# Performance work log

Measured on AMD Instinct MI355X. Metric: run time of the kernel, lower is better.

The kernel has to match this reference:

```python
import jax, jax.numpy as jnp
import numpy as np
from jax import lax

DIM = 128
HEADS = 8
HEAD_DIM = DIM // HEADS
SR = 2
B, H, W = 2, 80, 80
SCALE = HEAD_DIM ** (-0.5)
BN_EPS = 1e-5


def _conv1x1(x, w, b):
    # x: (B,C,H,W), w: (O,C), b: (O,)
    return jnp.einsum('bchw,oc->bohw', x, w) + b[None, :, None, None]


def setup_inputs() -> dict:
    key = jax.random.key(0)
    ks = jax.random.split(key, 12)
    s = DIM ** -0.5
    x = jax.random.normal(ks[0], (B, DIM, H, W), dtype=jnp.float32)
    q_w = jax.random.normal(ks[1], (DIM, DIM), dtype=jnp.float32) * s
    q_b = jnp.zeros((DIM,), jnp.float32)
    k_w = jax.random.normal(ks[2], (DIM, DIM), dtype=jnp.float32) * s
    k_b = jnp.zeros((DIM,), jnp.float32)
    v_w = jax.random.normal(ks[3], (DIM, DIM), dtype=jnp.float32) * s
    v_b = jnp.zeros((DIM,), jnp.float32)
    sr_w = jax.random.normal(ks[4], (DIM, DIM, SR, SR), dtype=jnp.float32) * (s / SR)
    sr_b = jnp.zeros((DIM,), jnp.float32)
    bn_gamma = jnp.ones((DIM,), jnp.float32)
    bn_beta = jnp.zeros((DIM,), jnp.float32)
    bn_mean = jnp.zeros((DIM,), jnp.float32)
    bn_var = jnp.ones((DIM,), jnp.float32)
    proj_w = jax.random.normal(ks[5], (DIM, DIM), dtype=jnp.float32) * s
    proj_b = jnp.zeros((DIM,), jnp.float32)
    return dict(x=x, q_w=q_w, q_b=q_b, k_w=k_w, k_b=k_b, v_w=v_w, v_b=v_b,
                sr_w=sr_w, sr_b=sr_b, bn_gamma=bn_gamma, bn_beta=bn_beta,
                bn_mean=bn_mean, bn_var=bn_var, proj_w=proj_w, proj_b=proj_b)


def reference(x, q_w, q_b, k_w, k_b, v_w, v_b, sr_w, sr_b,
              bn_gamma, bn_beta, bn_mean, bn_var, proj_w, proj_b):
    b, c, h, w = x.shape
    n = h * w
    # q: (B,h,N,d)
    q = _conv1x1(x, q_w, q_b).reshape(b, HEADS, HEAD_DIM, n).transpose(0, 1, 3, 2)
    # spatial reduction: Conv2d(k=SR, s=SR) + BN(eval) + ReLU
    x_kv = lax.conv_general_dilated(x, sr_w, window_strides=(SR, SR),
                                    padding='VALID',
                                    dimension_numbers=('NCHW', 'OIHW', 'NCHW'))
    x_kv = x_kv + sr_b[None, :, None, None]
    inv = bn_gamma / jnp.sqrt(bn_var + BN_EPS)
    x_kv = x_kv * inv[None, :, None, None] + (bn_beta - bn_mean * inv)[None, :, None, None]
    x_kv = jax.nn.relu(x_kv)
    n_kv = x_kv.shape[2] * x_kv.shape[3]
    k = _conv1x1(x_kv, k_w, k_b).reshape(b, HEADS, HEAD_DIM, n_kv).transpose(0, 1, 3, 2)
    v = _conv1x1(x_kv, v_w, v_b).reshape(b, HEADS, HEAD_DIM, n_kv).transpose(0, 1, 3, 2)
    # explicit attention: (B,h,N,N_kv)
    attn = jnp.einsum('bhnd,bhmd->bhnm', q, k) * SCALE
    attn = jax.nn.softmax(attn, axis=-1)
    out = jnp.einsum('bhnm,bhmd->bhnd', attn, v)  # (B,h,N,d)
    # faithful to source layout: transpose(1,2) then reshape to (B,C,H,W)
    out = out.transpose(0, 2, 1, 3).reshape(b, c, h, w)
    out = _conv1x1(out, proj_w, proj_b)
    return out
```

## Files before the change

### kernel.cpp

```cpp
#include <hip/hip_runtime.h>
#include <hip/hip_bf16.h>
#include <cmath>

#define DIM 128
#define HEADS 8
#define NBATCH 2
#define NQ 6400
#define NKV 1600
#define NC 50
#define BN_EPS 1e-5f
#define LOG2E 1.4426950408889634f

typedef __bf16 bf16_t;
typedef __attribute__((ext_vector_type(8))) __bf16 bf16x8;
typedef __attribute__((ext_vector_type(16))) float f32x16;

union BF8U { bf16x8 v; unsigned u[4]; };

__device__ inline unsigned packbf2(float a, float b) {
  union { __hip_bfloat162 v; unsigned u; } r;
  r.v = __float22bfloat162_rn(make_float2(a, b));
  return r.u;
}

__device__ inline unsigned short f2bf(float v) {
  unsigned u = __float_as_uint(v);
  return (unsigned short)((u + 0x7FFFu + ((u >> 16) & 1u)) >> 16);
}

__device__ inline bf16x8 ldw8(const float* __restrict__ p) {
  float4 w0 = *(const float4*)p;
  float4 w1 = *(const float4*)(p + 4);
  BF8U r;
  r.u[0] = packbf2(w0.x, w0.y);
  r.u[1] = packbf2(w0.z, w0.w);
  r.u[2] = packbf2(w1.x, w1.y);
  r.u[3] = packbf2(w1.z, w1.w);
  return r.v;
}

__global__ __launch_bounds__(256) void mgemm_qsr(
    const float* __restrict__ x,
    const float* __restrict__ q_w, const float* __restrict__ q_b,
    const float* __restrict__ sr_w, const float* __restrict__ sr_b,
    const float* __restrict__ bng, const float* __restrict__ bnb,
    const float* __restrict__ bnm, const float* __restrict__ bnv,
    unsigned short* __restrict__ Qb, unsigned short* __restrict__ xkvb,
    float sl)
{
  int t = threadIdx.x;
  int ln = t & 31, hf = (t >> 5) & 1, wid = t >> 6;
  int b = blockIdx.y;
  int o = wid * 32 + ln;
  f32x16 acc = {};

  if (blockIdx.x < 200) {
    int s0 = blockIdx.x * 32;
    const float* ab = x + (size_t)b * DIM * NQ + s0 + ln;
    const float* brow = q_w + (size_t)o * 128 + hf * 8;
#pragma unroll
    for (int c0 = 0; c0 < 128; c0 += 16) {
      BF8U af;
#pragma unroll
      for (int jj = 0; jj < 4; ++jj)
        af.u[jj] = packbf2(ab[(size_t)(c0 + hf * 8 + 2 * jj) * NQ],
                           ab[(size_t)(c0 + hf * 8 + 2 * jj + 1) * NQ]);
      acc = __builtin_amdgcn_mfma_f32_32x32x16_bf16(af.v, ldw8(&brow[c0]), acc, 0, 0, 0);
    }
    float bv = q_b[o];
#pragma unroll
    for (int g = 0; g < 4; ++g)
#pragma unroll
      for (int j = 0; j < 4; ++j) {
        int s = s0 + 8 * g + 4 * hf + j;
        Qb[((size_t)b * NQ + s) * DIM + o] = f2bf((acc[4 * g + j] + bv) * sl);
      }
  } else {
    int s0 = (blockIdx.x - 200) * 32;
    int m = s0 + ln;
    int i = m / 40, jp = m % 40;
    const float* ab = x + (size_t)b * DIM * NQ + i * 160 + 2 * jp;
    const float* brow = sr_w + (size_t)o * 512 + hf * 8;
#pragma unroll 4
    for (int c0 = 0; c0 < 512; c0 += 16) {
      BF8U af;
#pragma unroll
      for (int jj = 0; jj < 4; ++jj) {
        int ca = c0 + hf * 8 + 2 * jj, cb = ca + 1;
        float va_ = ab[(size_t)(ca >> 2) * NQ + ((ca >> 1) & 1) * 80 + (ca & 1)];
        float vb_ = ab[(size_t)(cb >> 2) * NQ + ((cb >> 1) & 1) * 80 + (cb & 1)];
        af.u[jj] = packbf2(va_, vb_);
      }
      acc = __builtin_amdgcn_mfma_f32_32x32x16_bf16(af.v, ldw8(&brow[c0]), acc, 0, 0, 0);
    }
    float bv = sr_b[o];
    float inv = bng[o] / sqrtf(bnv[o] + BN_EPS);
    float b2 = bnb[o] - bnm[o] * inv;
#pragma unroll
    for (int g = 0; g < 4; ++g)
#pragma unroll
      for (int j = 0; j < 4; ++j) {
        int s = s0 + 8 * g + 4 * hf + j;
        float v = fmaxf((acc[4 * g + j] + bv) * inv + b2, 0.f);
        xkvb[((size_t)b * NKV + s) * DIM + o] = f2bf(v);
      }
  }
}

__global__ __launch_bounds__(256) void mgemm_kv(
    const bf16_t* __restrict__ xkvb,
    const float* __restrict__ k_w, const float* __restrict__ k_b,
    const float* __restrict__ v_w, const float* __restrict__ v_b,
    unsigned short* __restrict__ Kp, unsigned short* __restrict__ Vp)
{
  int t = threadIdx.x;
  int ln = t & 31, hf = (t >> 5) & 1, wid = t >> 6;
  int b = blockIdx.y;
  int isv = blockIdx.z;
  int s0 = blockIdx.x * 32;
  const float* W = isv ? v_w : k_w;
  int o = wid * 32 + ln;

  const bf16_t* arow = &xkvb[((size_t)b * NKV + s0 + ln) * DIM + hf * 8];
  const float* brow = W + (size_t)o * DIM + hf * 8;
  f32x16 acc = {};
#pragma unroll
  for (int c0 = 0; c0 < 128; c0 += 16) {
    bf16x8 af = *(const bf16x8*)&arow[c0];
    acc = __builtin_amdgcn_mfma_f32_32x32x16_bf16(af, ldw8(&brow[c0]), acc, 0, 0, 0);
  }

  int hloc = o >> 4, d = o & 15;
  if (isv) {
    float bv = v_b[o];
    size_t CB = (((size_t)b * HEADS + hloc) * NC + (s0 >> 5)) * 1024;
    uint4 w0, w1;
    w0.x = packbf2(acc[0] + bv, acc[1] + bv);
    w0.y = packbf2(acc[2] + bv, acc[3] + bv);
    w0.z = packbf2(acc[4] + bv, acc[5] + bv);
    w0.w = packbf2(acc[6] + bv, acc[7] + bv);
    w1.x = packbf2(acc[8] + bv, acc[9] + bv);
    w1.y = packbf2(acc[10] + bv, acc[11] + bv);
    w1.z = packbf2(acc[12] + bv, acc[13] + bv);
    w1.w = packbf2(acc[14] + bv, acc[15] + bv);
    *(uint4*)&Vp[CB + d * 16 + hf * 8] = w0;
    *(uint4*)&Vp[CB + 512 + d * 16 + hf * 8] = w1;
    {
      int h2 = t >> 5, pos = t & 31;
      size_t CB2 = (((size_t)b * HEADS + h2) * NC + (s0 >> 5)) * 1024;
      Vp[CB2 + 256 + ((pos & 16) ? 512 : 0) + (pos & 15)] = 0x3F80;
    }
  } else {
    float bv = k_b[o];
    size_t CB = (((size_t)b * HEADS + hloc) * NC + (s0 >> 5)) * 512;
#pragma unroll
    for (int g = 0; g < 4; ++g)
#pragma unroll
      for (int j = 0; j < 4; ++j) {
        int sl2 = 8 * g + 4 * hf + j;
        Kp[CB + sl2 * 16 + d] = f2bf(acc[4 * g + j] + bv);
      }
  }
}

__global__ __launch_bounds__(256, 8) void attn_split(
    const bf16_t* __restrict__ Qb, const bf16_t* __restrict__ Kp,
    const bf16_t* __restrict__ Vp, unsigned short* __restrict__ Pb,
    float* __restrict__ Lsum, int nsplit)
{
  const int t = threadIdx.x;
  const int ln = t & 31, hf = (t >> 5) & 1, wid = t >> 6;
  const int h = blockIdx.y;
  const int b = blockIdx.z & 1, quarter = blockIdx.z >> 1;
  const int q0 = blockIdx.x * 128 + wid * 32;
  const int base = NC / nsplit, rem = NC % nsplit;
  const int kcnt = base + (quarter < rem ? 1 : 0);
  const int kstart = quarter * base + (quarter < rem ? quarter : rem);
  const int slice = quarter * 2 + b;

  bf16x8 qf = *(const bf16x8*)&Qb[((size_t)b * NQ + q0 + ln) * DIM + h * 16 + hf * 8];
  const int bh = b * HEADS + h;
  const bf16_t* kc = &Kp[((size_t)bh * NC + kstart) * 512 + ln * 16 + hf * 8];
  const bf16_t* vc = &Vp[((size_t)bh * NC + kstart) * 1024 + ln * 16 + hf * 8];

  f32x16 acc = {};
  const f32x16 zero = {};

  for (int c = 0; c < kcnt; ++c) {
    bf16x8 kf = *(const bf16x8*)kc;
    bf16x8 va = *(const bf16x8*)vc;
    bf16x8 vb = *(const bf16x8*)(vc + 512);

    f32x16 S = __builtin_amdgcn_mfma_f32_32x32x16_bf16(kf, qf, zero, 0, 0, 0);

    BF8U f0, f1;
#pragma unroll
    for (int i = 0; i < 4; ++i) {
      f0.u[i] = packbf2(__builtin_amdgcn_exp2f(S[2 * i]),
                        __builtin_amdgcn_exp2f(S[2 * i + 1]));
      f1.u[i] = packbf2(__builtin_amdgcn_exp2f(S[8 + 2 * i]),
                        __builtin_amdgcn_exp2f(S[9 + 2 * i]));
    }

    acc = __builtin_amdgcn_mfma_f32_32x32x16_bf16(va, f0.v, acc, 0, 0, 0);
    acc = __builtin_amdgcn_mfma_f32_32x32x16_bf16(vb, f1.v, acc, 0, 0, 0);
    kc += 512; vc += 1024;
  }

  unsigned short* prow =
      &Pb[(size_t)slice * (NQ * DIM) + (size_t)(q0 + ln) * DIM + h * 16 + 4 * hf];
  uint2 w0, w1;
  w0.x = packbf2(acc[0], acc[1]); w0.y = packbf2(acc[2], acc[3]);
  w1.x = packbf2(acc[4], acc[5]); w1.y = packbf2(acc[6], acc[7]);
  *(uint2*)&prow[0] = w0;
  *(uint2*)&prow[8] = w1;
  if (!hf)
    Lsum[(size_t)slice * (HEADS * NQ) + (size_t)h * NQ + q0 + ln] = acc[8];
}

__global__ __launch_bounds__(256) void proj_comb(
    const unsigned short* __restrict__ Pb, const float* __restrict__ Lsum,
    const float* __restrict__ p_w, const float* __restrict__ p_b,
    float* __restrict__ Out, int nsplit)
{
  __shared__ unsigned short As[32][136];
  int t = threadIdx.x;
  int b = blockIdx.y;
  int s0 = blockIdx.x * 32;

  {
    int tx = t & 31, cg = t >> 5;
#pragma unroll
    for (int it = 0; it < 16; ++it) {
      int c = cg * 16 + it;
      int f = c * NQ + s0 + tx;
      int n = f >> 7, hh = (f >> 4) & 7;
      float ps = 0.f, L = 0.f;
      for (int qq = 0; qq < nsplit; ++qq) {
        int sl2 = qq * 2 + b;
        ps += __uint_as_float((unsigned)Pb[(size_t)sl2 * (NQ * DIM) + f] << 16);
        L += Lsum[(size_t)sl2 * (HEADS * NQ) + (size_t)hh * NQ + n];
      }
      As[tx][c] = f2bf(ps / L);
    }
  }
  __syncthreads();

  int ln = t & 31, hf = (t >> 5) & 1, wid = t >> 6;
  int o = wid * 32 + ln;
  const float* brow = p_w + (size_t)o * DIM + hf * 8;
  const unsigned short* arow = &As[ln][hf * 8];
  f32x16 acc = {};
#pragma unroll
  for (int c0 = 0; c0 < 128; c0 += 16) {
    bf16x8 af = *(const bf16x8*)&arow[c0];
    acc = __builtin_amdgcn_mfma_f32_32x32x16_bf16(af, ldw8(&brow[c0]), acc, 0, 0, 0);
  }
  float bv = p_b[o];
  float* obase = &Out[((size_t)b * DIM + o) * NQ + s0 + 4 * hf];
#pragma unroll
  for (int g = 0; g < 4; ++g) {
    float4 r;
    r.x = acc[4 * g + 0] + bv; r.y = acc[4 * g + 1] + bv;
    r.z = acc[4 * g + 2] + bv; r.w = acc[4 * g + 3] + bv;
    *(float4*)&obase[8 * g] = r;
  }
}

extern "C" void kernel_launch(void* const* d_in, const int* in_sizes, int n_in,
                              void* d_out, int out_size, void* d_ws, size_t ws_size,
                              hipStream_t stream)
{
  const float* x    = (const float*)d_in[0];
  const float* q_w  = (const float*)d_in[1];
  const float* q_b  = (const float*)d_in[2];
  const float* k_w  = (const float*)d_in[3];
  const float* k_b  = (const float*)d_in[4];
  const float* v_w  = (const float*)d_in[5];
  const float* v_b  = (const float*)d_in[6];
  const float* sr_w = (const float*)d_in[7];
  const float* sr_b = (const float*)d_in[8];
  const float* bng  = (const float*)d_in[9];
  const float* bnb  = (const float*)d_in[10];
  const float* bnm  = (const float*)d_in[11];
  const float* bnv  = (const float*)d_in[12];
  const float* p_w  = (const float*)d_in[13];
  const float* p_b  = (const float*)d_in[14];
  float* out = (float*)d_out;

  const int nsplit = (ws_size >= (size_t)5120000 * 4) ? 4 : 2;

  float* ws = (float*)d_ws;
  bf16_t* Pb   = (bf16_t*)ws;
  bf16_t* xkvb = (bf16_t*)ws;
  size_t off = (size_t)nsplit * 819200;
  bf16_t* Qb = (bf16_t*)(ws + off);   off += 819200;
  bf16_t* Kp = (bf16_t*)(ws + off);   off += 204800;
  bf16_t* Vp = (bf16_t*)(ws + off);   off += 409600;
  float* Lsum = ws + off;

  const float sl = 0.25f * LOG2E;

  mgemm_qsr<<<dim3(250, NBATCH), dim3(256), 0, stream>>>(
      x, q_w, q_b, sr_w, sr_b, bng, bnb, bnm, bnv,
      (unsigned short*)Qb, (unsigned short*)xkvb, sl);

  mgemm_kv<<<dim3(NKV / 32, NBATCH, 2), dim3(256), 0, stream>>>(
      xkvb, k_w, k_b, v_w, v_b, (unsigned short*)Kp, (unsigned short*)Vp);

  attn_split<<<dim3(NQ / 128, HEADS, 2 * nsplit), dim3(256), 0, stream>>>(
      Qb, Kp, Vp, (unsigned short*)Pb, Lsum, nsplit);

  proj_comb<<<dim3(200, NBATCH), dim3(256), 0, stream>>>(
      (const unsigned short*)Pb, Lsum, p_w, p_b, out, nsplit);
}
```

Baseline: 168.6 us.

## Stage Q-proj input via LDS, vectorize SR loads, prefetch next KV chunk in attention

The Q projection branch now loads the x tile cooperatively with float4 reads, converts it to bf16 into shared memory, and then reads MFMA A-fragments as 16-byte LDS loads. This replaces scattered strided scalar global loads. The spatial-reduction branch merges each adjacent pixel pair into one float2 load. The attention loop software-prefetches the next chunk's K/V fragments into registers to hide global latency, which costs extra registers and adds a barrier in the projection kernel.

```diff
diff --git a/kernel.cpp b/kernel.cpp
--- a/kernel.cpp
+++ b/kernel.cpp
@@ -48,6 +48,7 @@
     unsigned short* __restrict__ Qb, unsigned short* __restrict__ xkvb,
     float sl)
 {
+  __shared__ __align__(16) unsigned short As[32][136];
   int t = threadIdx.x;
   int ln = t & 31, hf = (t >> 5) & 1, wid = t >> 6;
   int b = blockIdx.y;
@@ -56,16 +57,25 @@
 
   if (blockIdx.x < 200) {
     int s0 = blockIdx.x * 32;
-    const float* ab = x + (size_t)b * DIM * NQ + s0 + ln;
+    const float* xb = x + (size_t)b * DIM * NQ + s0;
+#pragma unroll
+    for (int it = 0; it < 4; ++it) {
+      int idx = t + it * 256;
+      int c = idx >> 3, s4 = (idx & 7) * 4;
+      float4 v = *(const float4*)&xb[(size_t)c * NQ + s4];
+      As[s4 + 0][c] = f2bf(v.x);
+      As[s4 + 1][c] = f2bf(v.y);
+      As[s4 + 2][c] = f2bf(v.z);
+      As[s4 + 3][c] = f2bf(v.w);
+    }
+    __syncthreads();
+
     const float* brow = q_w + (size_t)o * 128 + hf * 8;
+    const unsigned short* arow = &As[ln][hf * 8];
 #pragma unroll
     for (int c0 = 0; c0 < 128; c0 += 16) {
-      BF8U af;
-#pragma unroll
-      for (int jj = 0; jj < 4; ++jj)
-        af.u[jj] = packbf2(ab[(size_t)(c0 + hf * 8 + 2 * jj) * NQ],
-                           ab[(size_t)(c0 + hf * 8 + 2 * jj + 1) * NQ]);
-      acc = __builtin_amdgcn_mfma_f32_32x32x16_bf16(af.v, ldw8(&brow[c0]), acc, 0, 0, 0);
+      bf16x8 af = *(const bf16x8*)&arow[c0];
+      acc = __builtin_amdgcn_mfma_f32_32x32x16_bf16(af, ldw8(&brow[c0]), acc, 0, 0, 0);
     }
     float bv = q_b[o];
 #pragma unroll
@@ -86,10 +96,9 @@
       BF8U af;
 #pragma unroll
       for (int jj = 0; jj < 4; ++jj) {
-        int ca = c0 + hf * 8 + 2 * jj, cb = ca + 1;
-        float va_ = ab[(size_t)(ca >> 2) * NQ + ((ca >> 1) & 1) * 80 + (ca & 1)];
-        float vb_ = ab[(size_t)(cb >> 2) * NQ + ((cb >> 1) & 1) * 80 + (cb & 1)];
-        af.u[jj] = packbf2(va_, vb_);
+        int ca = c0 + hf * 8 + 2 * jj;
+        float2 v = *(const float2*)&ab[(size_t)(ca >> 2) * NQ + ((ca >> 1) & 1) * 80];
+        af.u[jj] = packbf2(v.x, v.y);
       }
       acc = __builtin_amdgcn_mfma_f32_32x32x16_bf16(af.v, ldw8(&brow[c0]), acc, 0, 0, 0);
     }
@@ -186,10 +195,15 @@
   f32x16 acc = {};
   const f32x16 zero = {};
 
+  bf16x8 kf = *(const bf16x8*)kc;
+  bf16x8 va = *(const bf16x8*)vc;
+  bf16x8 vb = *(const bf16x8*)(vc + 512);
+
   for (int c = 0; c < kcnt; ++c) {
-    bf16x8 kf = *(const bf16x8*)kc;
-    bf16x8 va = *(const bf16x8*)vc;
-    bf16x8 vb = *(const bf16x8*)(vc + 512);
+    int cn = (c + 1 < kcnt) ? c + 1 : c;
+    bf16x8 kf2 = *(const bf16x8*)(kc + cn * 512);
+    bf16x8 va2 = *(const bf16x8*)(vc + cn * 1024);
+    bf16x8 vb2 = *(const bf16x8*)(vc + cn * 1024 + 512);
 
     f32x16 S = __builtin_amdgcn_mfma_f32_32x32x16_bf16(kf, qf, zero, 0, 0, 0);
 
@@ -204,7 +218,7 @@
 
     acc = __builtin_amdgcn_mfma_f32_32x32x16_bf16(va, f0.v, acc, 0, 0, 0);
     acc = __builtin_amdgcn_mfma_f32_32x32x16_bf16(vb, f1.v, acc, 0, 0, 0);
-    kc += 512; vc += 1024;
+    kf = kf2; va = va2; vb = vb2;
   }
 
   unsigned short* prow =
@@ -223,7 +237,7 @@
     const float* __restrict__ p_w, const float* __restrict__ p_b,
     float* __restrict__ Out, int nsplit)
 {
-  __shared__ unsigned short As[32][136];
+  __shared__ __align__(16) unsigned short As[32][136];
   int t = threadIdx.x;
   int b = blockIdx.y;
   int s0 = blockIdx.x * 32;
```

Measured after the change: 170.4 us. Within noise of the previous version (+1.1%).
